# Kernel optimization log

Hardware: AMD Instinct MI355X
Metric: run time of the kernel (lower is better)

Reference implementation:

```python
import jax, jax.numpy as jnp
import numpy as np

NEG_SLOPE = 0.2  # LeakyReLU slope
PAD = 1          # padding for all 3x3 convs (kernel_size // 2)
K = 9            # 3x3 deformable kernel taps


def _conv2d(x, w, b):
    # x: (B,Cin,H,W), w: (Cout,Cin,3,3) -> (B,Cout,H,W), stride 1, SAME pad
    y = jax.lax.conv_general_dilated(x, w, (1, 1), 'SAME',
                                     dimension_numbers=('NCHW', 'OIHW', 'NCHW'))
    return y + b[None, :, None, None]


def _leaky(x):
    return jnp.where(x >= 0, x, NEG_SLOPE * x)


def _deform_conv(x, offset, w, b):
    # torchvision DeformConv2d, kernel 3x3, stride 1, pad 1, no modulation.
    # x: (B,C,H,W); offset: (B, 2*K, H, W) ordered (dy,dx) per tap; w: (O,C,3,3)
    B, C, H, W = x.shape
    O = w.shape[0]
    off = offset.reshape(B, K, 2, H, W)
    ks = jnp.arange(K)
    ky = (ks // 3).astype(x.dtype)
    kx = (ks % 3).astype(x.dtype)
    iy = jnp.arange(H, dtype=x.dtype)
    ix = jnp.arange(W, dtype=x.dtype)
    # sampling locations: out_pos + tap_pos - pad + learned offset  -> (B,K,H,W)
    py = iy[None, None, :, None] + ky[None, :, None, None] - PAD + off[:, :, 0]
    px = ix[None, None, None, :] + kx[None, :, None, None] - PAD + off[:, :, 1]

    y0 = jnp.floor(py)
    x0 = jnp.floor(px)
    wy = py - y0
    wx = px - x0
    y0i = y0.astype(jnp.int32)
    x0i = x0.astype(jnp.int32)

    def gather(img, yi, xi):  # img: (C,H,W); yi,xi: (K,H,W) -> (C,K,H,W)
        return img[:, yi, xi]
    vgather = jax.vmap(gather)  # over batch

    def corner(yi, xi, wgt):
        valid = (yi >= 0) & (yi < H) & (xi >= 0) & (xi < W)
        yc = jnp.clip(yi, 0, H - 1)
        xc = jnp.clip(xi, 0, W - 1)
        v = vgather(x, yc, xc)  # (B,C,K,H,W)
        return v * (wgt * valid.astype(x.dtype))[:, None]

    val = (corner(y0i, x0i, (1 - wy) * (1 - wx))
           + corner(y0i, x0i + 1, (1 - wy) * wx)
           + corner(y0i + 1, x0i, wy * (1 - wx))
           + corner(y0i + 1, x0i + 1, wy * wx))  # (B,C,K,H,W)
    out = jnp.einsum('bckhw,ock->bohw', val, w.reshape(O, C, K))
    return out + b[None, :, None, None]


def _stage(x, cw, cb, ow, ob, dw, db):
    h = _leaky(_conv2d(x, cw, cb))      # plain conv + LeakyReLU
    off = _conv2d(h, ow, ob)            # offset prediction (18 channels)
    return _leaky(_deform_conv(h, off, dw, db))


def setup_inputs() -> dict:
    key = jax.random.key(0)
    keys = iter(jax.random.split(key, 32))

    def nrm(shape, scale):
        return jax.random.normal(next(keys), shape, jnp.float32) * scale

    inp = {'x': jax.random.normal(next(keys), (4, 64, 128, 128), jnp.float32)}
    specs = [(64, 128), (128, 128), (128, 64)]
    for i, (ci, co) in enumerate(specs, 1):
        inp[f's{i}_cw'] = nrm((co, ci, 3, 3), (ci * 9) ** -0.5)
        inp[f's{i}_cb'] = jnp.zeros((co,), jnp.float32)
        inp[f's{i}_ow'] = nrm((18, co, 3, 3), 0.1 * (co * 9) ** -0.5)  # small offsets
        inp[f's{i}_ob'] = jnp.zeros((18,), jnp.float32)
        inp[f's{i}_dw'] = nrm((co, co, 3, 3), (co * 9) ** -0.5)
        inp[f's{i}_db'] = jnp.zeros((co,), jnp.float32)
    return inp


def reference(x,
              s1_cw, s1_cb, s1_ow, s1_ob, s1_dw, s1_db,
              s2_cw, s2_cb, s2_ow, s2_ob, s2_dw, s2_db,
              s3_cw, s3_cb, s3_ow, s3_ob, s3_dw, s3_db):
    x = _stage(x, s1_cw, s1_cb, s1_ow, s1_ob, s1_dw, s1_db)
    x = _stage(x, s2_cw, s2_cb, s2_ow, s2_ob, s2_dw, s2_db)
    x = _stage(x, s3_cw, s3_cb, s3_ow, s3_ob, s3_dw, s3_db)
    return x
```

## Files before the change

### kernel.cpp

```cpp
#include <hip/hip_runtime.h>
#include <hip/hip_bf16.h>

#define HW 128
#define HW2 16384
#define NEG 0.2f

typedef __attribute__((ext_vector_type(8))) short short8;
typedef __attribute__((ext_vector_type(4))) float f32x4;
typedef __attribute__((ext_vector_type(2))) float f32x2;

__device__ __forceinline__ float lrelu(float v) { return v >= 0.f ? v : NEG * v; }
__device__ __forceinline__ unsigned short f2bf(float f) {
    unsigned int u = __float_as_uint(f);
    u = (u + 0x7fffu + ((u >> 16) & 1u)) >> 16;
    return (unsigned short)u;
}
__device__ __forceinline__ unsigned int pk2(float a, float b) {
    __hip_bfloat162 h = __float22bfloat162_rn(float2{a, b});
    return *(unsigned int*)&h;
}
__device__ __forceinline__ float2 upk(unsigned int u) {
    return float2{__uint_as_float(u << 16), __uint_as_float(u & 0xffff0000u)};
}
__device__ __forceinline__ f32x2 upkv(unsigned int u) {
    f32x2 r;
    r.x = __uint_as_float(u << 16);
    r.y = __uint_as_float(u & 0xffff0000u);
    return r;
}

struct WSeg { const float* s; unsigned short* d; int K9; int NMT; int validM; int n; };
struct WArgs { WSeg seg[9]; };

__global__ void wrepack_kernel(WArgs a)
{
    const WSeg sg = a.seg[blockIdx.y];
    int i = blockIdx.x * 256 + threadIdx.x;
    if (i >= sg.n) return;
    int cl = i & 7, lane = (i >> 3) & 63;
    int rest = i >> 9;
    int mt = rest % sg.NMT, gs = rest / sg.NMT;
    int st = gs % 3, g = gs / 3;
    int quad = lane >> 4, l15 = lane & 15;
    int co = mt * 16 + l15, tap = st * 4 + quad;
    unsigned short v = 0;
    if (tap < 9 && co < sg.validM)
        v = f2bf(sg.s[(size_t)co * sg.K9 + (g * 8 + cl) * 9 + tap]);
    sg.d[i] = v;
}

template <int MTW, int SRCF>
__global__ __launch_bounds__(256, 4) void fused_conv(
    const void* __restrict__ actv, const unsigned short* __restrict__ wpad,
    const float* __restrict__ bias, unsigned short* __restrict__ outb,
    float* __restrict__ outf, int Cin, int Cout, int mode)
{
    constexpr int PB = 136 * 16;
    constexpr int SMB = 64 * 136 * 2;
    __shared__ char smem[SMB];
    unsigned short* Es = (unsigned short*)smem;

    const int t = threadIdx.x;
    const int tile = blockIdx.x, b = blockIdx.z;
    const int lane = t & 63, wv = t >> 6, quad = lane >> 4, l15 = lane & 15;
    const int y0 = (tile >> 2) * 2, x0 = (tile & 3) * 32;
    const int ngrp = Cin >> 3;
    const int NSTR = (Cout >> 4) * 512;

    const int pr = t / 34, pc = t - 34 * pr;
    const int gy = y0 - 1 + pr, gx = x0 - 1 + pc;
    const bool pok = (t < 136) && gy >= 0 && gy < HW && gx >= 0 && gx < HW;
    const int gp = pok ? gy * HW + gx : 0;

    const float* actf = (const float*)actv;
    const unsigned short* acth = (const unsigned short*)actv;
    const size_t bofs = (size_t)b * Cin * HW2;

    int baddr[3][4];
#pragma unroll
    for (int st = 0; st < 3; ++st) {
        int tap = st * 4 + quad; tap = tap > 8 ? 8 : tap;
        int ky = (tap * 11) >> 5, kx = tap - 3 * ky;
#pragma unroll
        for (int nt = 0; nt < 4; ++nt) {
            int p = nt * 16 + l15, ly = p >> 5, lx = p & 31;
            baddr[st][nt] = ((ly + ky) * 34 + lx + kx) * 16;
        }
    }
    size_t abase[MTW];
#pragma unroll
    for (int m = 0; m < MTW; ++m)
        abase[m] = (size_t)((wv * MTW + m) * 512 + lane * 8);

    f32x4 acc[MTW][4];
#pragma unroll
    for (int m = 0; m < MTW; ++m)
#pragma unroll
        for (int nt = 0; nt < 4; ++nt) acc[m][nt] = (f32x4)(0.f);

    auto load_grp = [&](int g) -> uint4 {
        uint4 u; u.x = u.y = u.z = u.w = 0;
        if (!pok) return u;
        if (SRCF == 1) {
            u = *(const uint4*)(acth + bofs + ((size_t)g * HW2 + gp) * 8);
        } else {
            const float* pl = actf + bofs + (size_t)(g * 8) * HW2 + gp;
            float v0 = pl[0], v1 = pl[HW2], v2 = pl[2 * HW2], v3 = pl[3 * HW2];
            float v4 = pl[4 * HW2], v5 = pl[5 * HW2], v6 = pl[6 * HW2], v7 = pl[7 * HW2];
            u.x = pk2(v0, v1); u.y = pk2(v2, v3);
            u.z = pk2(v4, v5); u.w = pk2(v6, v7);
        }
        return u;
    };

    short8 apre[MTW][3];
    auto loadA = [&](int g) {
#pragma unroll
        for (int st = 0; st < 3; ++st)
#pragma unroll
            for (int m = 0; m < MTW; ++m)
                apre[m][st] = *(const short8*)(wpad + (size_t)(g * 3 + st) * NSTR + abase[m]);
    };

    uint4 cur = load_grp(0);
    if (t < 136) *(uint4*)(smem + t * 16) = cur;
    loadA(0);
    if (ngrp > 1) cur = load_grp(1);
    __syncthreads();

    for (int g = 0; g < ngrp; ++g) {
        char* pb = smem + (g & 1) * PB;
#pragma unroll
        for (int st = 0; st < 3; ++st) {
            short8 bfr[4];
#pragma unroll
            for (int nt = 0; nt < 4; ++nt)
                bfr[nt] = *(const short8*)(pb + baddr[st][nt]);
#pragma unroll
            for (int m = 0; m < MTW; ++m) {
                short8 a = apre[m][st];
#pragma unroll
                for (int nt = 0; nt < 4; ++nt)
                    acc[m][nt] = __builtin_amdgcn_mfma_f32_16x16x32_bf16(
                        a, bfr[nt], acc[m][nt], 0, 0, 0);
            }
        }
        if (g + 1 < ngrp) {
            if (t < 136) *(uint4*)(smem + ((g + 1) & 1) * PB + t * 16) = cur;
            loadA(g + 1);
            if (g + 2 < ngrp) cur = load_grp(g + 2);
        }
        __syncthreads();
    }

    if (mode == 0) {
        constexpr int ESTR = 136;
#pragma unroll
        for (int m = 0; m < MTW; ++m) {
            int cb = (wv * MTW + m) * 16;
#pragma unroll
            for (int nt = 0; nt < 4; ++nt) {
                int px = nt * 16 + l15;
                int co = cb + quad * 4;
                unsigned int u0 = pk2(lrelu(acc[m][nt][0] + bias[co]),
                                      lrelu(acc[m][nt][1] + bias[co + 1]));
                unsigned int u1 = pk2(lrelu(acc[m][nt][2] + bias[co + 2]),
                                      lrelu(acc[m][nt][3] + bias[co + 3]));
                uint2 u; u.x = u0; u.y = u1;
                *(uint2*)&Es[px * ESTR + co] = u;
            }
        }
        __syncthreads();
        const int ng8 = Cout >> 3;
        unsigned short* ob = outb + (size_t)b * Cout * HW2;
        for (int tt = t; tt < 64 * ng8; tt += 256) {
            int cg = tt >> 6, px = tt & 63;
            int gp2 = (y0 + (px >> 5)) * HW + x0 + (px & 31);
            *(uint4*)(ob + ((size_t)cg * HW2 + gp2) * 8) =
                *(const uint4*)&Es[px * ESTR + cg * 8];
        }
    } else {
        float* of = outf + (size_t)b * 18 * HW2;
#pragma unroll
        for (int m = 0; m < MTW; ++m) {
            int cb = (wv * MTW + m) * 16;
#pragma unroll
            for (int nt = 0; nt < 4; ++nt) {
                int px = nt * 16 + l15;
                int gp2 = (y0 + (px >> 5)) * HW + x0 + (px & 31);
#pragma unroll
                for (int r = 0; r < 4; ++r) {
                    int co = cb + quad * 4 + r;
                    if (co < 18)
                        of[(size_t)co * HW2 + gp2] = acc[m][nt][r] + bias[co];
                }
            }
        }
    }
}

template <int MTW>
__global__ __launch_bounds__(256, 4) void fused_deform(
    const unsigned short* __restrict__ acth,
    const unsigned short* __restrict__ woff, const float* __restrict__ obias,
    const unsigned short* __restrict__ wpad, const float* __restrict__ bias,
    unsigned short* __restrict__ outb, float* __restrict__ outf,
    int Cin, int Cout, int mode)
{
    constexpr int PATW = 42, PATP = 420;
    constexpr int CSTR = 104;
    constexpr int PB = PATP * 16;
    constexpr int CB = 64 * CSTR * 2;
    constexpr int SMB = 2 * PB + 2 * CB;
    constexpr int OPB = 136 * 16;
    __shared__ char smem[SMB];
    unsigned short* Es = (unsigned short*)smem;

    const int t = threadIdx.x;
    const int tile = blockIdx.x, b = blockIdx.z;
    const int lane = t & 63, wv = t >> 6, quad = lane >> 4, l15 = lane & 15;
    const int y0 = (tile >> 2) * 2, x0 = (tile & 3) * 32;
    const int ngrp = Cin >> 3;
    const int NSTR = (Cout >> 4) * 512;
    const int py0 = y0 - 4, px0 = x0 - 4;
    const size_t bofs = (size_t)b * Cin * HW2;

    for (int i = t; i < 384; i += 256) {
        int bu = i / 192;
        int ii = i - 192 * bu;
        int p = ii / 3, j = ii - 3 * p;
        uint4 z; z.x = z.y = z.z = z.w = 0;
        *(uint4*)(smem + 2 * PB + bu * CB + (p * CSTR + 72 + j * 8) * 2) = z;
    }

    {
        float* offbuf = (float*)(smem + 2 * OPB);
        const int apr = t / 34, apc = t - 34 * apr;
        const int agy = y0 - 1 + apr, agx = x0 - 1 + apc;
        const bool apok = (t < 136) && agy >= 0 && agy < HW && agx >= 0 && agx < HW;
        const int agp = apok ? agy * HW + agx : 0;

        const int mtile = wv & 1, npair = wv >> 1;
        int obad[3][2];
#pragma unroll
        for (int st = 0; st < 3; ++st) {
            int tap = st * 4 + quad; tap = tap > 8 ? 8 : tap;
            int ky = (tap * 11) >> 5, kx = tap - 3 * ky;
#pragma unroll
            for (int nn = 0; nn < 2; ++nn) {
                int p = (2 * npair + nn) * 16 + l15, ly = p >> 5, lx = p & 31;
                obad[st][nn] = ((ly + ky) * 34 + lx + kx) * 16;
            }
        }
        const size_t oa0 = (size_t)(mtile * 512 + lane * 8);

        f32x4 oacc[2];
        oacc[0] = (f32x4)(0.f); oacc[1] = (f32x4)(0.f);
        short8 oapre[3];
        auto loadAO = [&](int g) {
#pragma unroll
            for (int st = 0; st < 3; ++st)
                oapre[st] = *(const short8*)(woff + (size_t)(g * 3 + st) * 1024 + oa0);
        };
        auto load_g = [&](int g) -> uint4 {
            uint4 u; u.x = u.y = u.z = u.w = 0;
            if (apok) u = *(const uint4*)(acth + bofs + ((size_t)g * HW2 + agp) * 8);
            return u;
        };

        uint4 cur = load_g(0);
        if (t < 136) *(uint4*)(smem + t * 16) = cur;
        loadAO(0);
        if (ngrp > 1) cur = load_g(1);
        __syncthreads();

        for (int g = 0; g < ngrp; ++g) {
            const char* pb = smem + (g & 1) * OPB;
#pragma unroll
            for (int st = 0; st < 3; ++st) {
                short8 a = oapre[st];
#pragma unroll
                for (int nn = 0; nn < 2; ++nn) {
                    short8 bf = *(const short8*)(pb + obad[st][nn]);
                    oacc[nn] = __builtin_amdgcn_mfma_f32_16x16x32_bf16(
                        a, bf, oacc[nn], 0, 0, 0);
                }
            }
            if (g + 1 < ngrp) {
                if (t < 136) *(uint4*)(smem + ((g + 1) & 1) * OPB + t * 16) = cur;
                loadAO(g + 1);
                if (g + 2 < ngrp) cur = load_g(g + 2);
            }
            __syncthreads();
        }

        {
            int co0 = mtile * 16 + quad * 4;
            if (co0 < 18) {
#pragma unroll
                for (int nn = 0; nn < 2; ++nn) {
                    int px = (2 * npair + nn) * 16 + l15;
#pragma unroll
                    for (int r = 0; r < 4; ++r)
                        if (co0 + r < 18)
                            offbuf[px * 20 + co0 + r] = oacc[nn][r] + obias[co0 + r];
                }
            }
        }
        __syncthreads();
    }
    const float* offbuf = (const float*)(smem + 2 * OPB);

    float w00[3], w01[3], w10[3], w11[3];
    int pbase[3], csad[3], svalid[3];
    int allin = 1;
    {
#pragma unroll
        for (int s = 0; s < 3; ++s) {
            int task = t + s * 256;
            svalid[s] = task < 576;
            int task2 = svalid[s] ? task : 0;
            int p = task2 / 9, k = task2 - 9 * p;
            int yy = y0 + (p >> 5), xx = x0 + (p & 31);
            float dy = offbuf[p * 20 + 2 * k];
            float dx = offbuf[p * 20 + 2 * k + 1];
            float py = (float)(yy + k / 3 - 1) + dy;
            float px = (float)(xx + k % 3 - 1) + dx;
            float fy = floorf(py), fx = floorf(px);
            float wy = py - fy, wx = px - fx;
            int iy = (int)fy, ix = (int)fx;
            w00[s] = (1.f - wy) * (1.f - wx);
            w01[s] = (1.f - wy) * wx;
            w10[s] = wy * (1.f - wx);
            w11[s] = wy * wx;
            pbase[s] = ((iy - py0) * PATW + (ix - px0)) * 16;
            csad[s] = (p * CSTR + k * 8) * 2;
            bool ip = iy >= py0 && iy + 1 <= y0 + 5 && ix >= px0 && ix + 1 <= x0 + 36;
            if (!ip) allin = 0;
        }
    }
    const int fast = __syncthreads_and(allin);

    const int r0 = t / PATW, c0_ = t - PATW * r0;
    const int gy0_ = py0 + r0, gx0_ = px0 + c0_;
    const bool ok0 = gy0_ >= 0 && gy0_ < HW && gx0_ >= 0 && gx0_ < HW;
    const int go0 = ok0 ? gy0_ * HW + gx0_ : 0;
    const int i1 = t + 256;
    const bool has1 = i1 < PATP;
    const int r1 = i1 / PATW, c1_ = i1 - PATW * r1;
    const int gy1_ = py0 + r1, gx1_ = px0 + c1_;
    const bool ok1 = has1 && gy1_ >= 0 && gy1_ < HW && gx1_ >= 0 && gx1_ < HW;
    const int go1 = ok1 ? gy1_ * HW + gx1_ : 0;

    size_t abase[MTW];
#pragma unroll
    for (int m = 0; m < MTW; ++m)
        abase[m] = (size_t)((wv * MTW + m) * 512 + lane * 8);
    const int bb0 = l15 * (CSTR * 2) + quad * 16;

    f32x4 acc[MTW][4];
#pragma unroll
    for (int m = 0; m < MTW; ++m)
#pragma unroll
        for (int nt = 0; nt < 4; ++nt) acc[m][nt] = (f32x4)(0.f);

    short8 apre[MTW][3];
    auto loadA = [&](int g) {
#pragma unroll
        for (int st = 0; st < 3; ++st)
#pragma unroll
            for (int m = 0; m < MTW; ++m)
                apre[m][st] = *(const short8*)(wpad + (size_t)(g * 3 + st) * NSTR + abase[m]);
    };

    auto mfma_pre = [&](const char* cs) {
#pragma unroll
        for (int st = 0; st < 3; ++st) {
            short8 bfr[4];
#pragma unroll
            for (int nt = 0; nt < 4; ++nt)
                bfr[nt] = *(const short8*)(cs + bb0 + nt * 16 * (CSTR * 2) + st * 64);
#pragma unroll
            for (int m = 0; m < MTW; ++m) {
                short8 a = apre[m][st];
#pragma unroll
                for (int nt = 0; nt < 4; ++nt)
                    acc[m][nt] = __builtin_amdgcn_mfma_f32_16x16x32_bf16(
                        a, bfr[nt], acc[m][nt], 0, 0, 0);
            }
        }
    };

    if (fast) {
        uint4 u0, u1;
        u0.x = u0.y = u0.z = u0.w = 0; u1 = u0;
        if (ok0) u0 = *(const uint4*)(acth + bofs + (size_t)go0 * 8);
        if (ok1) u1 = *(const uint4*)(acth + bofs + (size_t)go1 * 8);
        *(uint4*)(smem + t * 16) = u0;
        if (has1) *(uint4*)(smem + i1 * 16) = u1;
        if (ngrp > 1) {
            u0.x = u0.y = u0.z = u0.w = 0; u1 = u0;
            if (ok0) u0 = *(const uint4*)(acth + bofs + ((size_t)HW2 + go0) * 8);
            if (ok1) u1 = *(const uint4*)(acth + bofs + ((size_t)HW2 + go1) * 8);
        }
        __syncthreads();

        for (int g = 0; g < ngrp; ++g) {
            const char* pb = smem + (g & 1) * PB;
            char* csW = smem + 2 * PB + (g & 1) * CB;

            if (g > 0)
                mfma_pre(smem + 2 * PB + ((g - 1) & 1) * CB);

#pragma unroll
            for (int s = 0; s < 3; ++s) {
                if (!svalid[s]) continue;
                const char* base = pb + pbase[s];
                uint4 c00 = *(const uint4*)base;
                uint4 c01 = *(const uint4*)(base + 16);
                uint4 c10 = *(const uint4*)(base + PATW * 16);
                uint4 c11 = *(const uint4*)(base + PATW * 16 + 16);
                f32x2 vw0 = (f32x2)(w00[s]), vw1 = (f32x2)(w01[s]);
                f32x2 vw2 = (f32x2)(w10[s]), vw3 = (f32x2)(w11[s]);
                f32x2 a0 = vw0 * upkv(c00.x) + vw1 * upkv(c01.x)
                         + vw2 * upkv(c10.x) + vw3 * upkv(c11.x);
                f32x2 a1 = vw0 * upkv(c00.y) + vw1 * upkv(c01.y)
                         + vw2 * upkv(c10.y) + vw3 * upkv(c11.y);
                f32x2 a2 = vw0 * upkv(c00.z) + vw1 * upkv(c01.z)
                         + vw2 * upkv(c10.z) + vw3 * upkv(c11.z);
                f32x2 a3 = vw0 * upkv(c00.w) + vw1 * upkv(c01.w)
                         + vw2 * upkv(c10.w) + vw3 * upkv(c11.w);
                uint4 ou;
                ou.x = pk2(a0.x, a0.y); ou.y = pk2(a1.x, a1.y);
                ou.z = pk2(a2.x, a2.y); ou.w = pk2(a3.x, a3.y);
                *(uint4*)(csW + csad[s]) = ou;
            }

            if (g + 1 < ngrp) {
                char* pn = smem + ((g + 1) & 1) * PB;
                *(uint4*)(pn + t * 16) = u0;
                if (has1) *(uint4*)(pn + i1 * 16) = u1;
            }
            loadA(g);
            if (g + 2 < ngrp) {
                u0.x = u0.y = u0.z = u0.w = 0; u1 = u0;
                if (ok0) u0 = *(const uint4*)(acth + bofs +
                                              ((size_t)(g + 2) * HW2 + go0) * 8);
                if (ok1) u1 = *(const uint4*)(acth + bofs +
                                              ((size_t)(g + 2) * HW2 + go1) * 8);
            }
            __syncthreads();
        }
        mfma_pre(smem + 2 * PB + ((ngrp - 1) & 1) * CB);
    } else {
        char* csW = smem + 2 * PB;
        for (int g = 0; g < ngrp; ++g) {
            const unsigned short* gb = acth + bofs + (size_t)g * HW2 * 8;
#pragma unroll
            for (int s = 0; s < 3; ++s) {
                if (!svalid[s]) continue;
                int task = t + s * 256;
                int p = task / 9, k = task - 9 * p;
                int yy = y0 + (p >> 5), xx = x0 + (p & 31);
                float dy = offbuf[p * 20 + 2 * k];
                float dx = offbuf[p * 20 + 2 * k + 1];
                float py = (float)(yy + k / 3 - 1) + dy;
                float px = (float)(xx + k % 3 - 1) + dx;
                float fy = floorf(py), fx = floorf(px);
                float wy = py - fy, wx = px - fx;
                int iy = (int)fy, ix = (int)fx;
                float f0 = 0, f1 = 0, f2 = 0, f3 = 0, f4 = 0, f5 = 0, f6 = 0, f7 = 0;
#pragma unroll
                for (int q = 0; q < 4; ++q) {
                    int ddy = q >> 1, ddx = q & 1;
                    int sy = iy + ddy, sx = ix + ddx;
                    float w = (ddy ? wy : 1.f - wy) * (ddx ? wx : 1.f - wx);
                    if (sy < 0 || sy >= HW || sx < 0 || sx >= HW) w = 0.f;
                    int cy = min(max(sy, 0), HW - 1), cx = min(max(sx, 0), HW - 1);
                    uint4 c = *(const uint4*)(gb + (size_t)(cy * HW + cx) * 8);
                    float2 p0 = upk(c.x), p1 = upk(c.y), p2 = upk(c.z), p3 = upk(c.w);
                    f0 += w * p0.x; f1 += w * p0.y; f2 += w * p1.x; f3 += w * p1.y;
                    f4 += w * p2.x; f5 += w * p2.y; f6 += w * p3.x; f7 += w * p3.y;
                }
                uint4 ou;
                ou.x = pk2(f0, f1); ou.y = pk2(f2, f3);
                ou.z = pk2(f4, f5); ou.w = pk2(f6, f7);
                *(uint4*)(csW + csad[s]) = ou;
            }
            __syncthreads();
            loadA(g);
            mfma_pre(csW);
            __syncthreads();
        }
    }

    __syncthreads();
    if (mode == 0) {
        constexpr int ESTR = 136;
#pragma unroll
        for (int m = 0; m < MTW; ++m) {
            int cb = (wv * MTW + m) * 16;
#pragma unroll
            for (int nt = 0; nt < 4; ++nt) {
                int px = nt * 16 + l15;
                int co = cb + quad * 4;
                unsigned int u0 = pk2(lrelu(acc[m][nt][0] + bias[co]),
                                      lrelu(acc[m][nt][1] + bias[co + 1]));
                unsigned int u1 = pk2(lrelu(acc[m][nt][2] + bias[co + 2]),
                                      lrelu(acc[m][nt][3] + bias[co + 3]));
                uint2 u; u.x = u0; u.y = u1;
                *(uint2*)&Es[px * ESTR + co] = u;
            }
        }
        __syncthreads();
        const int ng8 = Cout >> 3;
        unsigned short* ob = outb + (size_t)b * Cout * HW2;
        for (int tt = t; tt < 64 * ng8; tt += 256) {
            int cg = tt >> 6, px = tt & 63;
            int gp2 = (y0 + (px >> 5)) * HW + x0 + (px & 31);
            *(uint4*)(ob + ((size_t)cg * HW2 + gp2) * 8) =
                *(const uint4*)&Es[px * ESTR + cg * 8];
        }
    } else {
        float* of = outf + (size_t)b * Cout * HW2;
#pragma unroll
        for (int m = 0; m < MTW; ++m) {
            int cb = (wv * MTW + m) * 16;
#pragma unroll
            for (int nt = 0; nt < 4; ++nt) {
                int px = nt * 16 + l15;
                int gp2 = (y0 + (px >> 5)) * HW + x0 + (px & 31);
#pragma unroll
                for (int r = 0; r < 4; ++r) {
                    int co = cb + quad * 4 + r;
                    of[(size_t)co * HW2 + gp2] = lrelu(acc[m][nt][r] + bias[co]);
                }
            }
        }
    }
}

extern "C" void kernel_launch(void* const* d_in, const int* in_sizes, int n_in,
                              void* d_out, int out_size, void* d_ws,
                              size_t ws_size, hipStream_t stream)
{
    const float* x = (const float*)d_in[0];
    const float* p[18];
    for (int i = 0; i < 18; ++i) p[i] = (const float*)d_in[1 + i];

    char* ws = (char*)d_ws;
    unsigned short* A1 = (unsigned short*)ws;
    unsigned short* A2 = (unsigned short*)(ws + 16777216);
    unsigned short* WB = (unsigned short*)(ws + 38273024);

    unsigned short* Wc1 = WB;
    unsigned short* Wo1 = Wc1 + 98304;
    unsigned short* Wd1 = Wo1 + 98304;
    unsigned short* Wc2 = Wd1 + 196608;
    unsigned short* Wo2 = Wc2 + 196608;
    unsigned short* Wd2 = Wo2 + 98304;
    unsigned short* Wc3 = Wd2 + 196608;
    unsigned short* Wo3 = Wc3 + 98304;
    unsigned short* Wd3 = Wo3 + 49152;

    WArgs wa;
    wa.seg[0] = {p[0],  Wc1,  576, 8, 128,  98304};
    wa.seg[1] = {p[2],  Wo1, 1152, 2,  18,  49152};
    wa.seg[2] = {p[4],  Wd1, 1152, 8, 128, 196608};
    wa.seg[3] = {p[6],  Wc2, 1152, 8, 128, 196608};
    wa.seg[4] = {p[8],  Wo2, 1152, 2,  18,  49152};
    wa.seg[5] = {p[10], Wd2, 1152, 8, 128, 196608};
    wa.seg[6] = {p[12], Wc3, 1152, 4,  64,  98304};
    wa.seg[7] = {p[14], Wo3,  576, 2,  18,  24576};
    wa.seg[8] = {p[16], Wd3,  576, 4,  64,  49152};
    wrepack_kernel<<<dim3(768, 9), 256, 0, stream>>>(wa);

    dim3 g(256, 1, 4);
    fused_conv<2, 0><<<g, 256, 0, stream>>>(x, Wc1, p[1], A1, nullptr, 64, 128, 0);
    fused_deform<2><<<g, 256, 0, stream>>>(A1, Wo1, p[3], Wd1, p[5], A2, nullptr, 128, 128, 0);
    fused_conv<2, 1><<<g, 256, 0, stream>>>(A2, Wc2, p[7], A1, nullptr, 128, 128, 0);
    fused_deform<2><<<g, 256, 0, stream>>>(A1, Wo2, p[9], Wd2, p[11], A2, nullptr, 128, 128, 0);
    fused_conv<1, 1><<<g, 256, 0, stream>>>(A2, Wc3, p[13], A1, nullptr, 128, 64, 0);
    fused_deform<1><<<g, 256, 0, stream>>>(A1, Wo3, p[15], Wd3, p[17], nullptr, (float*)d_out, 64, 64, 1);
}
```

Baseline: 302.9 us.

## Process two channel groups per barrier in conv and reshape deform patch

The plain conv loop now stages two 8-channel groups per iteration into a four-buffer shared layout, so all 256 threads take part in the halo loads and the number of __syncthreads calls is halved. Weight fragments for both groups are prefetched together, which raises register pressure. The deform kernel's shared patch changes from 10x42 to 8x43 with a shifted origin, which changes which offsets stay on the fast in-patch path. Offset pairs are also read with a single float2 load.

```diff
diff --git a/kernel.cpp b/kernel.cpp
--- a/kernel.cpp
+++ b/kernel.cpp
@@ -65,12 +65,21 @@
     const int lane = t & 63, wv = t >> 6, quad = lane >> 4, l15 = lane & 15;
     const int y0 = (tile >> 2) * 2, x0 = (tile & 3) * 32;
     const int ngrp = Cin >> 3;
+    const int P = ngrp >> 1;
     const int NSTR = (Cout >> 4) * 512;
 
-    const int pr = t / 34, pc = t - 34 * pr;
-    const int gy = y0 - 1 + pr, gx = x0 - 1 + pc;
-    const bool pok = (t < 136) && gy >= 0 && gy < HW && gx >= 0 && gx < HW;
-    const int gp = pok ? gy * HW + gx : 0;
+    const int ggA = t >= 136 ? 1 : 0;
+    const int idxA = t - ggA * 136;
+    const int prA = idxA / 34, pcA = idxA - 34 * prA;
+    const int gyA = y0 - 1 + prA, gxA = x0 - 1 + pcA;
+    const bool okA = gyA >= 0 && gyA < HW && gxA >= 0 && gxA < HW;
+    const int gpA = okA ? gyA * HW + gxA : 0;
+    const bool hasB = t < 16;
+    const int idxB = 120 + t;
+    const int prB = idxB / 34, pcB = idxB - 34 * prB;
+    const int gyB = y0 - 1 + prB, gxB = x0 - 1 + pcB;
+    const bool okB = hasB && gyB >= 0 && gyB < HW && gxB >= 0 && gxB < HW;
+    const int gpB = okB ? gyB * HW + gxB : 0;
 
     const float* actf = (const float*)actv;
     const unsigned short* acth = (const unsigned short*)actv;
@@ -98,9 +107,9 @@
 #pragma unroll
         for (int nt = 0; nt < 4; ++nt) acc[m][nt] = (f32x4)(0.f);
 
-    auto load_grp = [&](int g) -> uint4 {
+    auto load_one = [&](int g, int gp, bool ok) -> uint4 {
         uint4 u; u.x = u.y = u.z = u.w = 0;
-        if (!pok) return u;
+        if (!ok) return u;
         if (SRCF == 1) {
             u = *(const uint4*)(acth + bofs + ((size_t)g * HW2 + gp) * 8);
         } else {
@@ -113,42 +122,60 @@
         return u;
     };
 
-    short8 apre[MTW][3];
-    auto loadA = [&](int g) {
-#pragma unroll
-        for (int st = 0; st < 3; ++st)
-#pragma unroll
-            for (int m = 0; m < MTW; ++m)
-                apre[m][st] = *(const short8*)(wpad + (size_t)(g * 3 + st) * NSTR + abase[m]);
+    short8 apre[2][MTW][3];
+    auto loadApair = [&](int r) {
+#pragma unroll
+        for (int gg = 0; gg < 2; ++gg)
+#pragma unroll
+            for (int st = 0; st < 3; ++st)
+#pragma unroll
+                for (int m = 0; m < MTW; ++m)
+                    apre[gg][m][st] = *(const short8*)(
+                        wpad + (size_t)((2 * r + gg) * 3 + st) * NSTR + abase[m]);
     };
 
-    uint4 cur = load_grp(0);
-    if (t < 136) *(uint4*)(smem + t * 16) = cur;
-    loadA(0);
-    if (ngrp > 1) cur = load_grp(1);
+    uint4 cA = load_one(ggA, gpA, okA);
+    uint4 cB; cB.x = cB.y = cB.z = cB.w = 0;
+    if (hasB) cB = load_one(1, gpB, okB);
+    *(uint4*)(smem + ggA * PB + idxA * 16) = cA;
+    if (hasB) *(uint4*)(smem + PB + idxB * 16) = cB;
+    loadApair(0);
+    if (P > 1) {
+        cA = load_one(2 + ggA, gpA, okA);
+        if (hasB) cB = load_one(3, gpB, okB);
+    }
     __syncthreads();
 
-    for (int g = 0; g < ngrp; ++g) {
-        char* pb = smem + (g & 1) * PB;
-#pragma unroll
-        for (int st = 0; st < 3; ++st) {
-            short8 bfr[4];
-#pragma unroll
-            for (int nt = 0; nt < 4; ++nt)
-                bfr[nt] = *(const short8*)(pb + baddr[st][nt]);
-#pragma unroll
-            for (int m = 0; m < MTW; ++m) {
-                short8 a = apre[m][st];
+    for (int r = 0; r < P; ++r) {
+        const char* base = smem + (r & 1) * 2 * PB;
+#pragma unroll
+        for (int gg = 0; gg < 2; ++gg) {
+            const char* pb = base + gg * PB;
+#pragma unroll
+            for (int st = 0; st < 3; ++st) {
+                short8 bfr[4];
 #pragma unroll
                 for (int nt = 0; nt < 4; ++nt)
-                    acc[m][nt] = __builtin_amdgcn_mfma_f32_16x16x32_bf16(
-                        a, bfr[nt], acc[m][nt], 0, 0, 0);
-            }
-        }
-        if (g + 1 < ngrp) {
-            if (t < 136) *(uint4*)(smem + ((g + 1) & 1) * PB + t * 16) = cur;
-            loadA(g + 1);
-            if (g + 2 < ngrp) cur = load_grp(g + 2);
+                    bfr[nt] = *(const short8*)(pb + baddr[st][nt]);
+#pragma unroll
+                for (int m = 0; m < MTW; ++m) {
+                    short8 a = apre[gg][m][st];
+#pragma unroll
+                    for (int nt = 0; nt < 4; ++nt)
+                        acc[m][nt] = __builtin_amdgcn_mfma_f32_16x16x32_bf16(
+                            a, bfr[nt], acc[m][nt], 0, 0, 0);
+                }
+            }
+        }
+        if (r + 1 < P) {
+            char* nb = smem + ((r + 1) & 1) * 2 * PB;
+            *(uint4*)(nb + ggA * PB + idxA * 16) = cA;
+            if (hasB) *(uint4*)(nb + PB + idxB * 16) = cB;
+            loadApair(r + 1);
+            if (r + 2 < P) {
+                cA = load_one(2 * (r + 2) + ggA, gpA, okA);
+                if (hasB) cB = load_one(2 * (r + 2) + 1, gpB, okB);
+            }
         }
         __syncthreads();
     }
@@ -207,7 +234,7 @@
     unsigned short* __restrict__ outb, float* __restrict__ outf,
     int Cin, int Cout, int mode)
 {
-    constexpr int PATW = 42, PATP = 420;
+    constexpr int PATW = 43, PATR = 8, PATP = PATR * PATW;
     constexpr int CSTR = 104;
     constexpr int PB = PATP * 16;
     constexpr int CB = 64 * CSTR * 2;
@@ -222,7 +249,7 @@
     const int y0 = (tile >> 2) * 2, x0 = (tile & 3) * 32;
     const int ngrp = Cin >> 3;
     const int NSTR = (Cout >> 4) * 512;
-    const int py0 = y0 - 4, px0 = x0 - 4;
+    const int py0 = y0 - 3, px0 = x0 - 5;
     const size_t bofs = (size_t)b * Cin * HW2;
 
     for (int i = t; i < 384; i += 256) {
@@ -322,8 +349,8 @@
             int task2 = svalid[s] ? task : 0;
             int p = task2 / 9, k = task2 - 9 * p;
             int yy = y0 + (p >> 5), xx = x0 + (p & 31);
-            float dy = offbuf[p * 20 + 2 * k];
-            float dx = offbuf[p * 20 + 2 * k + 1];
+            float2 dd = *(const float2*)(offbuf + p * 20 + 2 * k);
+            float dy = dd.x, dx = dd.y;
             float py = (float)(yy + k / 3 - 1) + dy;
             float px = (float)(xx + k % 3 - 1) + dx;
             float fy = floorf(py), fx = floorf(px);
@@ -335,7 +362,8 @@
             w11[s] = wy * wx;
             pbase[s] = ((iy - py0) * PATW + (ix - px0)) * 16;
             csad[s] = (p * CSTR + k * 8) * 2;
-            bool ip = iy >= py0 && iy + 1 <= y0 + 5 && ix >= px0 && ix + 1 <= x0 + 36;
+            bool ip = iy >= py0 && iy + 1 <= py0 + (PATR - 1)
+                   && ix >= px0 && ix + 1 <= px0 + (PATW - 1);
             if (!ip) allin = 0;
         }
     }
@@ -462,8 +490,8 @@
                 int task = t + s * 256;
                 int p = task / 9, k = task - 9 * p;
                 int yy = y0 + (p >> 5), xx = x0 + (p & 31);
-                float dy = offbuf[p * 20 + 2 * k];
-                float dx = offbuf[p * 20 + 2 * k + 1];
+                float2 dd = *(const float2*)(offbuf + p * 20 + 2 * k);
+                float dy = dd.x, dx = dd.y;
                 float py = (float)(yy + k / 3 - 1) + dy;
                 float px = (float)(xx + k % 3 - 1) + dx;
                 float fy = floorf(py), fx = floorf(px);
```

Measured after the change: 332.3 us. 9.7% more time.
